# Optimization experiments

Hardware: AMD Instinct MI355X
Metric: run time of the kernel (lower is better)

The kernel has to match this reference:

```python
import jax, jax.numpy as jnp
import numpy as np

# ---- static config derived from init_kwargs ----
MIN_RES = np.array([16, 16, 16], dtype=np.float64)
MAX_RES = np.array([512, 512, 512], dtype=np.float64)
NUM_SCALES = 16
TABLE_SIZE = 2 ** 19          # max_params per level (power of two)
F = 2                          # features_per_level
N_QUERIES = 1_000_000

# per-axis geometric growth factor between levels (instant-ngp)
_B = np.exp((np.log(MAX_RES) - np.log(MIN_RES)) / (NUM_SCALES - 1))
RES = [np.floor(MIN_RES * _B ** l).astype(np.int64) for l in range(NUM_SCALES)]

PRIMES = np.array([1, 2654435761, 805459861], dtype=np.uint32)
# 8 corner offsets of the unit cube, [8,3]
OFFS = np.stack(np.meshgrid([0, 1], [0, 1], [0, 1], indexing='ij'), -1).reshape(8, 3)


def _level_encode(x, tab, res):
    """x: [N,3] in [0,1]; tab: [T,F]; res: static int64[3]. Returns [N,F]."""
    scaled = x * jnp.asarray(res.astype(np.float32))          # [N,3]
    pos0 = jnp.floor(scaled)
    w = scaled - pos0                                          # trilinear weights, [N,3]
    corners = pos0.astype(jnp.uint32)[:, None, :] + jnp.asarray(OFFS, jnp.uint32)[None]  # [N,8,3]
    n_cells = int((res[0] + 1) * (res[1] + 1) * (res[2] + 1))
    if n_cells <= TABLE_SIZE:
        # dense (non-hashed) indexing for coarse levels that fit in the table
        stride = np.array([1, res[0] + 1, (res[0] + 1) * (res[1] + 1)], dtype=np.uint32)
        idx = (corners * jnp.asarray(stride)).sum(-1)          # [N,8]
    else:
        # spatial hash: xor of coord*prime, mod table size
        cp = corners * jnp.asarray(PRIMES)
        idx = (cp[..., 0] ^ cp[..., 1] ^ cp[..., 2]) % jnp.uint32(TABLE_SIZE)
    feats = tab[idx.astype(jnp.int32)]                         # [N,8,F] gather
    offs_f = jnp.asarray(OFFS, x.dtype)                        # [8,3]
    # weight of each corner = prod over axes of (w if offset==1 else 1-w)
    wc = jnp.prod(jnp.where(offs_f[None] == 1, w[:, None, :], 1 - w[:, None, :]), axis=-1)  # [N,8]
    return jnp.einsum('nc,ncf->nf', wc, feats)                 # [N,F]


def setup_inputs() -> dict:
    key = jax.random.key(0)
    kx, kt = jax.random.split(key)
    x = jax.random.uniform(kx, (N_QUERIES, 3), dtype=jnp.float32)
    # instant-ngp initializes hash features uniform in [-1e-4, 1e-4]
    table = jax.random.uniform(kt, (NUM_SCALES, TABLE_SIZE, F), dtype=jnp.float32,
                               minval=-1e-4, maxval=1e-4)
    return {"x": x, "table": table}


def reference(x, table):
    outs = [_level_encode(x, table[l], RES[l]) for l in range(NUM_SCALES)]
    return jnp.concatenate(outs, axis=-1)                      # [N, NUM_SCALES*F]
```

## Files before the change

### kernel.cpp

```cpp
#include <hip/hip_runtime.h>
#include <cmath>

#define NLEV 16
#define TSZ  (1u << 19)
#define TMASK (TSZ - 1u)
#define PR1 2654435761u
#define PR2 805459861u
#define NBUCK 32768

struct LvlP {
    float    rf[NLEV];
    unsigned s1[NLEV];
    unsigned s2[NLEV];
};

static __device__ __forceinline__ unsigned part1by2(unsigned x) {
    x &= 0x3FFu;
    x = (x | (x << 16)) & 0x030000FFu;
    x = (x | (x << 8))  & 0x0300F00Fu;
    x = (x | (x << 4))  & 0x030C30C3u;
    x = (x | (x << 2))  & 0x09249249u;
    return x;
}
static __device__ __forceinline__ unsigned bucket_of(float x0, float x1, float x2) {
    unsigned bx = min(31u, (unsigned)(x0 * 32.0f));
    unsigned by = min(31u, (unsigned)(x1 * 32.0f));
    unsigned bz = min(31u, (unsigned)(x2 * 32.0f));
    return part1by2(bx) | (part1by2(by) << 1) | (part1by2(bz) << 2);
}
static __device__ __forceinline__ unsigned short f2bf(float f) {
    unsigned u = __float_as_uint(f);
    unsigned r = ((u >> 16) & 1u) + 0x7FFFu;
    return (unsigned short)((u + r) >> 16);
}
static __device__ __forceinline__ float bf2f(unsigned short h) {
    return __uint_as_float(((unsigned)h) << 16);
}

__global__ __launch_bounds__(256) void zero_pos_kernel(unsigned* __restrict__ pos) {
    pos[blockIdx.x * 256 + threadIdx.x] = 0u;
}

__global__ __launch_bounds__(256) void hist_kernel(
    const float* __restrict__ xs, unsigned* __restrict__ pos, int n)
{
    int i = blockIdx.x * 256 + threadIdx.x;
    if (i >= n) return;
    unsigned b = bucket_of(xs[3 * i], xs[3 * i + 1], xs[3 * i + 2]);
    atomicAdd(&pos[b], 1u);
}

__global__ __launch_bounds__(256) void scanA_kernel(
    unsigned* __restrict__ pos, unsigned* __restrict__ bsum)
{
    __shared__ unsigned sh[256];
    int t = threadIdx.x;
    int g = blockIdx.x * 256 + t;
    unsigned v = pos[g];
    sh[t] = v;
    __syncthreads();
    for (int off = 1; off < 256; off <<= 1) {
        unsigned u = (t >= off) ? sh[t - off] : 0u;
        __syncthreads();
        sh[t] += u;
        __syncthreads();
    }
    pos[g] = sh[t] - v;
    if (t == 255) bsum[blockIdx.x] = sh[255];
}

__global__ __launch_bounds__(128) void scanB_kernel(unsigned* __restrict__ bsum)
{
    __shared__ unsigned sh[128];
    int t = threadIdx.x;
    unsigned v = bsum[t];
    sh[t] = v;
    __syncthreads();
    for (int off = 1; off < 128; off <<= 1) {
        unsigned u = (t >= off) ? sh[t - off] : 0u;
        __syncthreads();
        sh[t] += u;
        __syncthreads();
    }
    bsum[t] = sh[t] - v;
}

__global__ __launch_bounds__(256) void scanC_kernel(
    unsigned* __restrict__ pos, const unsigned* __restrict__ bsum)
{
    int g = blockIdx.x * 256 + threadIdx.x;
    pos[g] += bsum[blockIdx.x];
}

__global__ __launch_bounds__(256) void scatter_kernel(
    const float* __restrict__ xs, unsigned* __restrict__ pos,
    float4* __restrict__ S, int n)
{
    int i = blockIdx.x * 256 + threadIdx.x;
    if (i >= n) return;
    float x0 = xs[3 * i], x1 = xs[3 * i + 1], x2 = xs[3 * i + 2];
    unsigned b = bucket_of(x0, x1, x2);
    unsigned j = atomicAdd(&pos[b], 1u);
    S[j] = make_float4(x0, x1, x2, __uint_as_float((unsigned)i));
}

template <bool DENSE>
static __device__ __forceinline__ ushort2 enc_one(
    float x0, float x1, float x2, float rf, unsigned st1, unsigned st2,
    unsigned lbase, const float4* __restrict__ t4)
{
    float s0 = x0 * rf, s1f = x1 * rf, s2f = x2 * rf;
    float p0 = floorf(s0), p1 = floorf(s1f), p2 = floorf(s2f);
    float w0 = s0 - p0, w1 = s1f - p1, w2 = s2f - p2;
    unsigned c0 = (unsigned)p0, c1 = (unsigned)p1, c2 = (unsigned)p2;

    float2 f[8];
    #pragma unroll
    for (int p = 0; p < 4; ++p) {
        unsigned oy = (p >> 1) & 1u, oz = p & 1u;
        unsigned q0, q1;
        if (DENSE) {
            unsigned b = c0 + (c1 + oy) * st1 + (c2 + oz) * st2;
            q0 = b; q1 = b + 1u;
        } else {
            unsigned h = ((c1 + oy) * PR1) ^ ((c2 + oz) * PR2);
            q0 = (h ^ c0) & TMASK;
            q1 = (h ^ (c0 + 1u)) & TMASK;
        }
        float4 v0 = t4[(lbase + (q0 & ~1u)) >> 1];
        float2 e0 = make_float2(v0.x, v0.y), e1 = make_float2(v0.z, v0.w);
        float2 fa = (q0 & 1u) ? e1 : e0;
        bool one = DENSE ? ((q0 & 1u) == 0u) : ((c0 & 1u) == 0u);
        float2 fb;
        if (one) {
            fb = (q0 & 1u) ? e0 : e1;
        } else {
            float4 v1 = t4[(lbase + (q1 & ~1u)) >> 1];
            fb = (q1 & 1u) ? make_float2(v1.z, v1.w) : make_float2(v1.x, v1.y);
        }
        f[p] = fa;
        f[p + 4] = fb;
    }

    float i0w = 1.f - w0, i1w = 1.f - w1, i2w = 1.f - w2;
    float acc0 = 0.f, acc1 = 0.f;
    #pragma unroll
    for (int k = 0; k < 8; ++k) {
        float wa = ((k >> 2) & 1) ? w0 : i0w;
        float wb = ((k >> 1) & 1) ? w1 : i1w;
        float wcv = (k & 1) ? w2 : i2w;
        float wk = (wa * wb) * wcv;
        acc0 = fmaf(wk, f[k].x, acc0);
        acc1 = fmaf(wk, f[k].y, acc1);
    }
    return make_ushort2(f2bf(acc0), f2bf(acc1));
}

__global__ __launch_bounds__(256) void enc_kernel(
    const float4* __restrict__ S, const float* __restrict__ table,
    ushort2* __restrict__ F, int n, int C, LvlP lp)
{
    int bid = blockIdx.x;
    int u = bid / C;
    int chunk = bid - u * C;
    int j = chunk * 256 + (int)threadIdx.x;
    if (j >= n) return;

    float4 s4 = S[j];
    float x0 = s4.x, x1 = s4.y, x2 = s4.z;
    const float4* __restrict__ t4 = (const float4*)table;

    if (u == 0) {
        #pragma unroll
        for (int l = 0; l < 7; ++l) {
            ushort2 r = enc_one<true>(x0, x1, x2, lp.rf[l], lp.s1[l], lp.s2[l],
                                      (unsigned)l << 19, t4);
            F[(size_t)l * n + j] = r;
        }
    } else {
        int l = u + 6;
        ushort2 r = enc_one<false>(x0, x1, x2, lp.rf[l], 0u, 0u,
                                   (unsigned)l << 19, t4);
        F[(size_t)l * n + j] = r;
    }
}

__global__ __launch_bounds__(256) void tr_scatter_kernel(
    const ushort2* __restrict__ F, const float4* __restrict__ S,
    float4* __restrict__ out4, int n)
{
    __shared__ ushort2 tile[16][65];
    __shared__ unsigned sorig[64];
    int t = threadIdx.x;
    int base = blockIdx.x * 64;
    int p  = t & 63;
    int l0 = t >> 6;
    #pragma unroll
    for (int r = 0; r < 4; ++r) {
        int l = l0 * 4 + r;
        int gi = base + p;
        if (gi < n) tile[l][p] = F[(size_t)l * n + gi];
    }
    if (t < 64 && base + t < n) sorig[t] = __float_as_uint(S[base + t].w);
    __syncthreads();
    #pragma unroll
    for (int r = 0; r < 2; ++r) {
        int idx = t + 256 * r;
        int pp = idx >> 3;
        int q  = idx & 7;
        int gi = base + pp;
        if (gi < n) {
            ushort2 a = tile[2 * q][pp];
            ushort2 b = tile[2 * q + 1][pp];
            out4[(size_t)sorig[pp] * 8 + q] =
                make_float4(bf2f(a.x), bf2f(a.y), bf2f(b.x), bf2f(b.y));
        }
    }
}

__global__ __launch_bounds__(256) void hashenc_kernel(
    const float* __restrict__ xs, const float* __restrict__ table,
    float* __restrict__ out, int n, LvlP lp)
{
    int i = blockIdx.x * 256 + threadIdx.x;
    if (i >= n) return;
    float x0 = xs[3 * i], x1 = xs[3 * i + 1], x2 = xs[3 * i + 2];
    const float2* __restrict__ t2 = (const float2*)table;
    float2* __restrict__ o2 = (float2*)out;
    #pragma unroll
    for (int l = 0; l < NLEV; ++l) {
        float rf = lp.rf[l];
        float s0 = x0 * rf, s1f = x1 * rf, s2f = x2 * rf;
        float p0 = floorf(s0), p1 = floorf(s1f), p2 = floorf(s2f);
        float w0 = s0 - p0, w1 = s1f - p1, w2 = s2f - p2;
        unsigned c0 = (unsigned)p0, c1 = (unsigned)p1, c2 = (unsigned)p2;
        float2 f[8];
        #pragma unroll
        for (int k = 0; k < 8; ++k) {
            unsigned a0 = c0 + ((k >> 2) & 1u), a1 = c1 + ((k >> 1) & 1u), a2 = c2 + (k & 1u);
            unsigned id;
            if (l < 7) id = a0 + a1 * lp.s1[l] + a2 * lp.s2[l];
            else       id = (a0 ^ (a1 * PR1) ^ (a2 * PR2)) & TMASK;
            f[k] = t2[((unsigned)l << 19) + id];
        }
        float i0 = 1.f - w0, i1 = 1.f - w1, i2 = 1.f - w2;
        float acc0 = 0.f, acc1 = 0.f;
        #pragma unroll
        for (int k = 0; k < 8; ++k) {
            float wa = ((k >> 2) & 1) ? w0 : i0;
            float wb = ((k >> 1) & 1) ? w1 : i1;
            float wcv = (k & 1) ? w2 : i2;
            float wk = (wa * wb) * wcv;
            acc0 = fmaf(wk, f[k].x, acc0);
            acc1 = fmaf(wk, f[k].y, acc1);
        }
        o2[(size_t)i * 16 + l] = make_float2(acc0, acc1);
    }
}

extern "C" void kernel_launch(void* const* d_in, const int* in_sizes, int n_in,
                              void* d_out, int out_size, void* d_ws, size_t ws_size,
                              hipStream_t stream)
{
    const float* xs    = (const float*)d_in[0];
    const float* table = (const float*)d_in[1];
    float* out = (float*)d_out;
    int n = in_sizes[0] / 3;

    LvlP lp;
    double B = exp((log(512.0) - log(16.0)) / 15.0);
    for (int l = 0; l < NLEV; ++l) {
        double rd;
        if (l == 0)      rd = 16.0;
        else if (l == 1) rd = floor(16.0 * B);
        else if (l == 2) rd = floor(16.0 * (B * B));
        else             rd = floor(16.0 * pow(B, (double)l));
        unsigned r = (unsigned)rd;
        lp.rf[l] = (float)r;
        lp.s1[l] = r + 1u;
        lp.s2[l] = (r + 1u) * (r + 1u);
    }

    int C = (n + 255) / 256;
    size_t posB  = (size_t)NBUCK * 4;
    size_t bsumB = 1024;
    size_t sB    = (size_t)n * 16;
    size_t fB    = (size_t)NLEV * (size_t)n * 4;
    size_t need  = posB + bsumB + sB + fB;

    if (ws_size >= need) {
        char* wsc = (char*)d_ws;
        unsigned* pos  = (unsigned*)wsc;
        unsigned* bsum = (unsigned*)(wsc + posB);
        float4*   S    = (float4*)(wsc + posB + bsumB);
        ushort2*  F    = (ushort2*)(wsc + posB + bsumB + sB);

        zero_pos_kernel<<<NBUCK / 256, 256, 0, stream>>>(pos);
        hist_kernel<<<C, 256, 0, stream>>>(xs, pos, n);
        scanA_kernel<<<NBUCK / 256, 256, 0, stream>>>(pos, bsum);
        scanB_kernel<<<1, 128, 0, stream>>>(bsum);
        scanC_kernel<<<NBUCK / 256, 256, 0, stream>>>(pos, bsum);
        scatter_kernel<<<C, 256, 0, stream>>>(xs, pos, S, n);
        enc_kernel<<<10 * C, 256, 0, stream>>>(S, table, F, n, C, lp);
        tr_scatter_kernel<<<(n + 63) / 64, 256, 0, stream>>>(F, S, (float4*)out, n);
    } else {
        hashenc_kernel<<<C, 256, 0, stream>>>(xs, table, out, n, lp);
    }
}
```

Baseline: 353.8 us.

## Fuse per-level encoding with output scatter into one kernel per point

Replaces the level-split encoding kernel plus the transpose-scatter kernel with one kernel. Each thread computes all 16 levels for a sorted point and writes its 32 floats directly to the original output row. This drops the bf16 intermediate buffer and its write/read round trip, and it removes the bf16 rounding of the output. In exchange the grid is ten times smaller and each thread runs all levels serially, so there is less parallelism for hiding gather latency and register pressure is higher.

Result: slower. 533.1 us (+50.7%).

```diff
diff --git a/kernel.cpp b/kernel.cpp
--- a/kernel.cpp
+++ b/kernel.cpp
@@ -27,14 +27,6 @@
     unsigned by = min(31u, (unsigned)(x1 * 32.0f));
     unsigned bz = min(31u, (unsigned)(x2 * 32.0f));
     return part1by2(bx) | (part1by2(by) << 1) | (part1by2(bz) << 2);
-}
-static __device__ __forceinline__ unsigned short f2bf(float f) {
-    unsigned u = __float_as_uint(f);
-    unsigned r = ((u >> 16) & 1u) + 0x7FFFu;
-    return (unsigned short)((u + r) >> 16);
-}
-static __device__ __forceinline__ float bf2f(unsigned short h) {
-    return __uint_as_float(((unsigned)h) << 16);
 }
 
 __global__ __launch_bounds__(256) void zero_pos_kernel(unsigned* __restrict__ pos) {
@@ -105,7 +97,7 @@
 }
 
 template <bool DENSE>
-static __device__ __forceinline__ ushort2 enc_one(
+static __device__ __forceinline__ float2 enc_one(
     float x0, float x1, float x2, float rf, unsigned st1, unsigned st2,
     unsigned lbase, const float4* __restrict__ t4)
 {
@@ -153,69 +145,39 @@
         acc0 = fmaf(wk, f[k].x, acc0);
         acc1 = fmaf(wk, f[k].y, acc1);
     }
-    return make_ushort2(f2bf(acc0), f2bf(acc1));
-}
-
-__global__ __launch_bounds__(256) void enc_kernel(
+    return make_float2(acc0, acc1);
+}
+
+__global__ __launch_bounds__(256) void enc_fused_kernel(
     const float4* __restrict__ S, const float* __restrict__ table,
-    ushort2* __restrict__ F, int n, int C, LvlP lp)
-{
-    int bid = blockIdx.x;
-    int u = bid / C;
-    int chunk = bid - u * C;
-    int j = chunk * 256 + (int)threadIdx.x;
+    float4* __restrict__ out4, int n, LvlP lp)
+{
+    int j = blockIdx.x * 256 + (int)threadIdx.x;
     if (j >= n) return;
 
     float4 s4 = S[j];
     float x0 = s4.x, x1 = s4.y, x2 = s4.z;
+    unsigned orig = __float_as_uint(s4.w);
     const float4* __restrict__ t4 = (const float4*)table;
 
-    if (u == 0) {
-        #pragma unroll
-        for (int l = 0; l < 7; ++l) {
-            ushort2 r = enc_one<true>(x0, x1, x2, lp.rf[l], lp.s1[l], lp.s2[l],
-                                      (unsigned)l << 19, t4);
-            F[(size_t)l * n + j] = r;
-        }
-    } else {
-        int l = u + 6;
-        ushort2 r = enc_one<false>(x0, x1, x2, lp.rf[l], 0u, 0u,
-                                   (unsigned)l << 19, t4);
-        F[(size_t)l * n + j] = r;
-    }
-}
-
-__global__ __launch_bounds__(256) void tr_scatter_kernel(
-    const ushort2* __restrict__ F, const float4* __restrict__ S,
-    float4* __restrict__ out4, int n)
-{
-    __shared__ ushort2 tile[16][65];
-    __shared__ unsigned sorig[64];
-    int t = threadIdx.x;
-    int base = blockIdx.x * 64;
-    int p  = t & 63;
-    int l0 = t >> 6;
-    #pragma unroll
-    for (int r = 0; r < 4; ++r) {
-        int l = l0 * 4 + r;
-        int gi = base + p;
-        if (gi < n) tile[l][p] = F[(size_t)l * n + gi];
-    }
-    if (t < 64 && base + t < n) sorig[t] = __float_as_uint(S[base + t].w);
-    __syncthreads();
-    #pragma unroll
-    for (int r = 0; r < 2; ++r) {
-        int idx = t + 256 * r;
-        int pp = idx >> 3;
-        int q  = idx & 7;
-        int gi = base + pp;
-        if (gi < n) {
-            ushort2 a = tile[2 * q][pp];
-            ushort2 b = tile[2 * q + 1][pp];
-            out4[(size_t)sorig[pp] * 8 + q] =
-                make_float4(bf2f(a.x), bf2f(a.y), bf2f(b.x), bf2f(b.y));
-        }
-    }
+    float acc[32];
+    #pragma unroll
+    for (int l = 0; l < 7; ++l) {
+        float2 r = enc_one<true>(x0, x1, x2, lp.rf[l], lp.s1[l], lp.s2[l],
+                                 (unsigned)l << 19, t4);
+        acc[2 * l] = r.x; acc[2 * l + 1] = r.y;
+    }
+    #pragma unroll
+    for (int l = 7; l < NLEV; ++l) {
+        float2 r = enc_one<false>(x0, x1, x2, lp.rf[l], 0u, 0u,
+                                  (unsigned)l << 19, t4);
+        acc[2 * l] = r.x; acc[2 * l + 1] = r.y;
+    }
+
+    float4* __restrict__ dst = out4 + (size_t)orig * 8;
+    #pragma unroll
+    for (int q = 0; q < 8; ++q)
+        dst[q] = make_float4(acc[4 * q], acc[4 * q + 1], acc[4 * q + 2], acc[4 * q + 3]);
 }
 
 __global__ __launch_bounds__(256) void hashenc_kernel(
@@ -285,15 +247,13 @@
     size_t posB  = (size_t)NBUCK * 4;
     size_t bsumB = 1024;
     size_t sB    = (size_t)n * 16;
-    size_t fB    = (size_t)NLEV * (size_t)n * 4;
-    size_t need  = posB + bsumB + sB + fB;
+    size_t need  = posB + bsumB + sB;
 
     if (ws_size >= need) {
         char* wsc = (char*)d_ws;
         unsigned* pos  = (unsigned*)wsc;
         unsigned* bsum = (unsigned*)(wsc + posB);
         float4*   S    = (float4*)(wsc + posB + bsumB);
-        ushort2*  F    = (ushort2*)(wsc + posB + bsumB + sB);
 
         zero_pos_kernel<<<NBUCK / 256, 256, 0, stream>>>(pos);
         hist_kernel<<<C, 256, 0, stream>>>(xs, pos, n);
@@ -301,8 +261,7 @@
         scanB_kernel<<<1, 128, 0, stream>>>(bsum);
         scanC_kernel<<<NBUCK / 256, 256, 0, stream>>>(pos, bsum);
         scatter_kernel<<<C, 256, 0, stream>>>(xs, pos, S, n);
-        enc_kernel<<<10 * C, 256, 0, stream>>>(S, table, F, n, C, lp);
-        tr_scatter_kernel<<<(n + 63) / 64, 256, 0, stream>>>(F, S, (float4*)out, n);
+        enc_fused_kernel<<<C, 256, 0, stream>>>(S, table, (float4*)out, n, lp);
     } else {
         hashenc_kernel<<<C, 256, 0, stream>>>(xs, table, out, n, lp);
     }
```
